# Kernel tuning notes

Measured on AMD Instinct MI355X. Metric: run time of the kernel, lower is better.

The kernel has to match this reference:

```python
import jax, jax.numpy as jnp
import numpy as np

N = 100000      # nodes
E = 3200000     # directed edges
F_IN = 128      # input node features
H = 16          # hidden width (fixed by module code)
C = 40          # classes
K_HOPS = 10
ALPHA = 0.1
BN_EPS = 1e-5


def gcn_conv(x, W, b, src, dst, n):
    """PyG GCNConv: add self-loops, symmetric D^-1/2 (A+I) D^-1/2 aggregation of x@W, plus bias."""
    loop = jnp.arange(n)
    s = jnp.concatenate([src, loop])
    d = jnp.concatenate([dst, loop])
    deg = jax.ops.segment_sum(jnp.ones(s.shape[0], x.dtype), d, num_segments=n)
    dinv = jnp.where(deg > 0, jax.lax.rsqrt(deg), 0.0)
    norm = dinv[s] * dinv[d]                      # [E+N]
    h = x @ W                                     # [N, out]
    out = jax.ops.segment_sum(h[s] * norm[:, None], d, num_segments=n)
    return out + b


def setup_inputs() -> dict:
    key = jax.random.key(0)
    ks = jax.random.split(key, 6)
    x = jax.random.normal(ks[0], (N, F_IN), jnp.float32)
    src = jax.random.randint(ks[1], (E,), 0, N)
    dst = jax.random.randint(ks[2], (E,), 0, N)
    glorot = lambda k, sh, fan: jax.random.normal(k, sh, jnp.float32) * np.float32(1.0 / np.sqrt(fan))
    W1 = glorot(ks[3], (F_IN, H), F_IN)
    b1 = jnp.zeros((H,), jnp.float32)
    gamma = jnp.ones((H,), jnp.float32)
    beta = jnp.zeros((H,), jnp.float32)
    Wl = glorot(ks[4], (H, H), H)
    bl = jnp.zeros((H,), jnp.float32)
    W2 = glorot(ks[5], (H, C), H)
    b2 = jnp.zeros((C,), jnp.float32)
    return dict(x=x, src=src, dst=dst, W1=W1, b1=b1, gamma=gamma, beta=beta,
                Wl=Wl, bl=bl, W2=W2, b2=b2)


def reference(x, src, dst, W1, b1, gamma, beta, Wl, bl, W2, b2):
    h = jax.nn.relu(gcn_conv(x, W1, b1, src, dst, N))
    # BatchNorm1d in training mode: biased batch statistics over nodes
    mean = h.mean(axis=0)
    var = h.var(axis=0)
    h = (h - mean) * jax.lax.rsqrt(var + BN_EPS) * gamma + beta
    # k_hops iterations of tiny linear-relu-residual blend
    def step(h, _):
        return ALPHA * jax.nn.relu(h @ Wl + bl) + (1.0 - ALPHA) * h, None
    h, _ = jax.lax.scan(step, h, None, length=K_HOPS)
    out = gcn_conv(h, W2, b2, src, dst, N)
    return jax.nn.log_softmax(out, axis=1)
```

## Files before the change

kernel.cpp:

```cpp
#include <hip/hip_runtime.h>
#include <hip/hip_fp16.h>
#include <math.h>

#define F_IN 128
#define H 16
#define C 40
#define K_HOPS 10
#define ALPHA 0.1f
#define BN_EPS 1e-5f

#define RB 256
#define RB_BITS 8
#define NBKT_MAX 512
#define SRC_MASK 0x1FFFF
#define PADQ 32
#define NDUMMY 2048
#define CAPB_BITS 14
#define CAPB (1 << CAPB_BITS)
#define STAGE_CAP 14336

typedef int v4i __attribute__((ext_vector_type(4)));

__global__ void k_zero(int* __restrict__ gcur, float* __restrict__ stats,
                       __half* __restrict__ h1h, __half* __restrict__ hh, int n) {
    int id = blockIdx.x * blockDim.x + threadIdx.x;
    if (id < NBKT_MAX) gcur[id] = id << CAPB_BITS;
    if (id < 32) stats[id] = 0.0f;
    int* z1 = (int*)(h1h + (size_t)n * H);
    int* z2 = (int*)(hh + (size_t)n * H);
    if (id < NDUMMY * H / 2) { z1[id] = 0; z2[id] = 0; }
}

#define BIN_CHUNK 2048
__global__ __launch_bounds__(256) void k_bin(const int* __restrict__ src,
                                             const int* __restrict__ dst,
                                             int* __restrict__ gcur,
                                             int* __restrict__ temp, int e) {
    __shared__ int hist[NBKT_MAX];
    __shared__ int lcur[NBKT_MAX];
    int t = threadIdx.x;
    hist[t] = 0; hist[t + 256] = 0;
    __syncthreads();
    int base = blockIdx.x * BIN_CHUNK;
    int ss[8], dd[8];
#pragma unroll
    for (int i = 0; i < 8; ++i) {
        int idx = base + i * 256 + t;
        if (idx < e) {
            ss[i] = src[idx]; dd[i] = dst[idx];
            atomicAdd(&hist[dd[i] >> RB_BITS], 1);
        } else ss[i] = -1;
    }
    __syncthreads();
    for (int b = t; b < NBKT_MAX; b += 256) {
        int hv = hist[b];
        lcur[b] = hv ? atomicAdd(&gcur[b], hv) : 0;
    }
    __syncthreads();
#pragma unroll
    for (int i = 0; i < 8; ++i) {
        if (ss[i] >= 0) {
            int d = dd[i];
            int b = d >> RB_BITS;
            int pos = atomicAdd(&lcur[b], 1);
            temp[pos] = ss[i] | ((d & (RB - 1)) << 17);
        }
    }
}

__global__ __launch_bounds__(256) void k_sort(const int* __restrict__ gcur,
                                              const int* __restrict__ temp,
                                              int* __restrict__ csr,
                                              int* __restrict__ ostart,
                                              int* __restrict__ oend,
                                              int* __restrict__ onode,
                                              float* __restrict__ dinv, int n) {
    __shared__ int hist[RB];
    __shared__ int cur[RB];
    __shared__ int psum[256];
    __shared__ int qh[64];
    __shared__ int qb[64];
    __shared__ int stage[STAGE_CAP];
    int t = threadIdx.x;
    int bkt = blockIdx.x;
    int start = bkt << CAPB_BITS;
    int endi = gcur[bkt];
    hist[t] = 0;
    if (t < 64) qh[t] = 0;
    __syncthreads();
    for (int k = start + t; k < endi; k += 2048) {
        int v[8];
#pragma unroll
        for (int i = 0; i < 8; ++i) { int ix = k + i * 256; v[i] = (ix < endi) ? temp[ix] : -1; }
#pragma unroll
        for (int i = 0; i < 8; ++i) if (v[i] >= 0) atomicAdd(&hist[v[i] >> 17], 1);
    }
    __syncthreads();
    int node = (bkt << RB_BITS) + t;
    int h = hist[t];
    int p = (h + PADQ - 1) & ~(PADQ - 1);
    bool va = (node < n);
    if (va) dinv[node] = rsqrtf((float)(h + 1));
    psum[t] = p;
    __syncthreads();
    for (int off = 1; off < 256; off <<= 1) {
        int tmp = (t >= off) ? psum[t - off] : 0;
        __syncthreads();
        psum[t] += tmp;
        __syncthreads();
    }
    int pexcl = psum[t] - p;
    int s0 = start + pexcl;
    int q = 63 - min(p >> 5, 63);
    int r = atomicAdd(&qh[q], 1);
    __syncthreads();
    int ptotal = psum[255];
    if (t == 0) {
        int run = 0;
        for (int i = 0; i < 64; ++i) { qb[i] = run; run += qh[i]; }
    }
    __syncthreads();
    int ga = (bkt << RB_BITS) + qb[q] + r;
    ostart[ga] = s0; oend[ga] = s0 + p; onode[ga] = va ? node : -1;

    if (ptotal <= STAGE_CAP) {
        cur[t] = pexcl;
        for (int i = t; i < ptotal; i += 256) stage[i] = -1;
        __syncthreads();
        for (int k = start + t; k < endi; k += 2048) {
            int v[8];
#pragma unroll
            for (int i = 0; i < 8; ++i) { int ix = k + i * 256; v[i] = (ix < endi) ? temp[ix] : -1; }
#pragma unroll
            for (int i = 0; i < 8; ++i) {
                if (v[i] >= 0) {
                    int pos = atomicAdd(&cur[v[i] >> 17], 1);
                    stage[pos] = v[i] & SRC_MASK;
                }
            }
        }
        __syncthreads();
        for (int i = t * 4; i < ptotal; i += 1024) {
            v4i v = *reinterpret_cast<const v4i*>(&stage[i]);
            int gi = start + i;
            v.x = (v.x < 0) ? n + ((gi + 0) & (NDUMMY - 1)) : v.x;
            v.y = (v.y < 0) ? n + ((gi + 1) & (NDUMMY - 1)) : v.y;
            v.z = (v.z < 0) ? n + ((gi + 2) & (NDUMMY - 1)) : v.z;
            v.w = (v.w < 0) ? n + ((gi + 3) & (NDUMMY - 1)) : v.w;
            *reinterpret_cast<v4i*>(&csr[gi]) = v;
        }
    } else {
        cur[t] = s0;
        __syncthreads();
        for (int k = start + t; k < endi; k += 256) {
            int v = temp[k];
            int pos = atomicAdd(&cur[v >> 17], 1);
            csr[pos] = v & SRC_MASK;
        }
        __syncthreads();
        for (int i = s0 + h; i < s0 + p; ++i) csr[i] = n + (i & (NDUMMY - 1));
    }
}

__global__ __launch_bounds__(256) void k_mm1(const float* __restrict__ x,
                                             const float* __restrict__ W1,
                                             const float* __restrict__ dinv,
                                             __half* __restrict__ h1h, int n) {
    __shared__ __align__(16) float xs[16 * 132];
    __shared__ __align__(16) float ws[128 * 16];
    int t = threadIdx.x;
    int node0 = blockIdx.x * 16;
    const float4* x4 = reinterpret_cast<const float4*>(x);
    const float4* w4 = reinterpret_cast<const float4*>(W1);
#pragma unroll
    for (int r = 0; r < 2; ++r) {
        int f = t + r * 256;
        int nl = f >> 5, k4 = f & 31;
        int nn = node0 + nl; if (nn >= n) nn = n - 1;
        *reinterpret_cast<float4*>(&xs[nl * 132 + k4 * 4]) = x4[(size_t)nn * 32 + k4];
        *reinterpret_cast<float4*>(&ws[f * 4]) = w4[f];
    }
    __syncthreads();
    int nl = t >> 4, j = t & 15;
    float acc = 0.0f;
#pragma unroll 8
    for (int k = 0; k < 128; ++k)
        acc = fmaf(xs[nl * 132 + k], ws[k * 16 + j], acc);
    int node = node0 + nl;
    if (node < n) h1h[(size_t)node * H + j] = __float2half(acc * dinv[node]);
}

__device__ __forceinline__ void acc8(float* a, int4 gv) {
    const __half2* h = reinterpret_cast<const __half2*>(&gv);
    float2 f0 = __half22float2(h[0]);
    float2 f1 = __half22float2(h[1]);
    float2 f2 = __half22float2(h[2]);
    float2 f3 = __half22float2(h[3]);
    a[0] += f0.x; a[1] += f0.y; a[2] += f1.x; a[3] += f1.y;
    a[4] += f2.x; a[5] += f2.y; a[6] += f3.x; a[7] += f3.y;
}

__global__ __launch_bounds__(256) void k_gather1(const int* __restrict__ ostart,
                                                 const int* __restrict__ oend,
                                                 const int* __restrict__ onode,
                                                 const int* __restrict__ csr,
                                                 const __half* __restrict__ h1h,
                                                 const float* __restrict__ dinv,
                                                 const float* __restrict__ b1,
                                                 float* __restrict__ hout,
                                                 float* __restrict__ stats, int n) {
    __shared__ float sm[32];
    __shared__ float b1s[16];
    int t = threadIdx.x;
    if (t < 32) sm[t] = 0.0f;
    if (t < 16) b1s[t] = b1[t];
    __syncthreads();
    int idx = blockIdx.x * 256 + t;
    int g = idx >> 2;
    int L = idx & 3, p = L >> 1, jj = L & 1;
    int node = __builtin_nontemporal_load(onode + g);
    float a[8];
#pragma unroll
    for (int k = 0; k < 8; ++k) a[k] = 0.0f;
    const int4* tab = reinterpret_cast<const int4*>(h1h);
    if (node >= 0) {
        int c  = (__builtin_nontemporal_load(ostart + g) >> 2) + (p << 2);
        int ce = __builtin_nontemporal_load(oend + g) >> 2;
        const v4i* csr4 = reinterpret_cast<const v4i*>(csr);
        for (; c < ce; c += 8) {
            v4i e0 = __builtin_nontemporal_load(csr4 + c);
            v4i e1 = __builtin_nontemporal_load(csr4 + c + 1);
            v4i e2 = __builtin_nontemporal_load(csr4 + c + 2);
            v4i e3 = __builtin_nontemporal_load(csr4 + c + 3);
            int4 g0  = tab[(size_t)e0.x * 2 + jj];
            int4 g1  = tab[(size_t)e0.y * 2 + jj];
            int4 g2  = tab[(size_t)e0.z * 2 + jj];
            int4 g3  = tab[(size_t)e0.w * 2 + jj];
            int4 g4  = tab[(size_t)e1.x * 2 + jj];
            int4 g5  = tab[(size_t)e1.y * 2 + jj];
            int4 g6  = tab[(size_t)e1.z * 2 + jj];
            int4 g7  = tab[(size_t)e1.w * 2 + jj];
            int4 g8  = tab[(size_t)e2.x * 2 + jj];
            int4 g9  = tab[(size_t)e2.y * 2 + jj];
            int4 g10 = tab[(size_t)e2.z * 2 + jj];
            int4 g11 = tab[(size_t)e2.w * 2 + jj];
            int4 g12 = tab[(size_t)e3.x * 2 + jj];
            int4 g13 = tab[(size_t)e3.y * 2 + jj];
            int4 g14 = tab[(size_t)e3.z * 2 + jj];
            int4 g15 = tab[(size_t)e3.w * 2 + jj];
            acc8(a, g0);  acc8(a, g1);  acc8(a, g2);  acc8(a, g3);
            acc8(a, g4);  acc8(a, g5);  acc8(a, g6);  acc8(a, g7);
            acc8(a, g8);  acc8(a, g9);  acc8(a, g10); acc8(a, g11);
            acc8(a, g12); acc8(a, g13); acc8(a, g14); acc8(a, g15);
        }
    }
#pragma unroll
    for (int k = 0; k < 8; ++k) a[k] += __shfl_xor(a[k], 2);
    float din = 0.0f;
    int4 sv = make_int4(0, 0, 0, 0);
    if (node >= 0) {
        din = dinv[node];
        sv = tab[(size_t)node * 2 + jj];
    }
    float v[8];
    {
        const __half2* h = reinterpret_cast<const __half2*>(&sv);
        float2 f0 = __half22float2(h[0]), f1 = __half22float2(h[1]);
        float2 f2 = __half22float2(h[2]), f3 = __half22float2(h[3]);
        float s8[8] = { f0.x, f0.y, f1.x, f1.y, f2.x, f2.y, f3.x, f3.y };
        bool writer = (node >= 0) && (p == 0);
#pragma unroll
        for (int k = 0; k < 8; ++k) {
            float val = fmaxf(din * (a[k] + s8[k]) + b1s[jj * 8 + k], 0.0f);
            v[k] = writer ? val : 0.0f;
        }
        if (writer) {
            float4* o = reinterpret_cast<float4*>(hout + (size_t)node * H + jj * 8);
            o[0] = make_float4(v[0], v[1], v[2], v[3]);
            o[1] = make_float4(v[4], v[5], v[6], v[7]);
        }
    }
#pragma unroll
    for (int k = 0; k < 8; ++k) {
        float s1 = v[k], s2 = v[k] * v[k];
        s1 += __shfl_xor(s1, 2);  s2 += __shfl_xor(s2, 2);
        s1 += __shfl_xor(s1, 4);  s2 += __shfl_xor(s2, 4);
        s1 += __shfl_xor(s1, 8);  s2 += __shfl_xor(s2, 8);
        s1 += __shfl_xor(s1, 16); s2 += __shfl_xor(s2, 16);
        s1 += __shfl_xor(s1, 32); s2 += __shfl_xor(s2, 32);
        if ((t & 63) < 2) {
            atomicAdd(&sm[jj * 8 + k], s1);
            atomicAdd(&sm[16 + jj * 8 + k], s2);
        }
    }
    __syncthreads();
    if (t < 32) atomicAdd(&stats[t], sm[t]);
}

__global__ void k_bncoef(float* __restrict__ stats, const float* __restrict__ gamma,
                         const float* __restrict__ beta, float nf) {
    int j = threadIdx.x;
    if (j < 16) {
        float mean = stats[j] / nf;
        float var = stats[16 + j] / nf - mean * mean;
        float a = gamma[j] * rsqrtf(var + BN_EPS);
        float c = beta[j] - mean * a;
        stats[j] = a;
        stats[16 + j] = c;
    }
}

__global__ __launch_bounds__(256) void k_hops(const float* __restrict__ h,
                                              __half* __restrict__ hh,
                                              const float* __restrict__ stats,
                                              const float* __restrict__ Wl,
                                              const float* __restrict__ bl,
                                              const float* __restrict__ dinv, int n) {
    __shared__ float wl[256], bls[16], av[16], cv[16];
    int t = threadIdx.x;
    wl[t] = Wl[(t & 15) * 16 + (t >> 4)];
    if (t < 16) { bls[t] = bl[t]; av[t] = stats[t]; cv[t] = stats[16 + t]; }
    __syncthreads();
    int node = blockIdx.x * 256 + t;
    if (node >= n) return;
    float hr[16];
    {
        const float4* hp = reinterpret_cast<const float4*>(h + (size_t)node * H);
        float4 v0 = hp[0], v1 = hp[1], v2 = hp[2], v3 = hp[3];
        hr[0] = v0.x; hr[1] = v0.y; hr[2] = v0.z; hr[3] = v0.w;
        hr[4] = v1.x; hr[5] = v1.y; hr[6] = v1.z; hr[7] = v1.w;
        hr[8] = v2.x; hr[9] = v2.y; hr[10] = v2.z; hr[11] = v2.w;
        hr[12] = v3.x; hr[13] = v3.y; hr[14] = v3.z; hr[15] = v3.w;
    }
#pragma unroll
    for (int j = 0; j < 16; ++j) hr[j] = hr[j] * av[j] + cv[j];
    for (int it = 0; it < K_HOPS; ++it) {
        float tmp[16];
#pragma unroll
        for (int j = 0; j < 16; ++j) {
            float a = bls[j];
#pragma unroll
            for (int k = 0; k < 16; ++k) a = fmaf(hr[k], wl[j * 16 + k], a);
            tmp[j] = fmaxf(a, 0.0f);
        }
#pragma unroll
        for (int j = 0; j < 16; ++j) hr[j] = ALPHA * tmp[j] + (1.0f - ALPHA) * hr[j];
    }
    {
        float din = dinv[node];
        __half2 ph[8];
#pragma unroll
        for (int i = 0; i < 8; ++i)
            ph[i] = __floats2half2_rn(hr[2 * i] * din, hr[2 * i + 1] * din);
        int4* hp = reinterpret_cast<int4*>(hh + (size_t)node * H);
        hp[0] = *reinterpret_cast<int4*>(&ph[0]);
        hp[1] = *reinterpret_cast<int4*>(&ph[4]);
    }
}

__global__ __launch_bounds__(256) void k_gather2(const int* __restrict__ ostart,
                                                 const int* __restrict__ oend,
                                                 const int* __restrict__ onode,
                                                 const int* __restrict__ csr,
                                                 const __half* __restrict__ hh,
                                                 const float* __restrict__ dinv,
                                                 float* __restrict__ agg, int n) {
    int t = threadIdx.x;
    int idx = blockIdx.x * 256 + t;
    int g = idx >> 2;
    int L = idx & 3, p = L >> 1, jj = L & 1;
    int node = __builtin_nontemporal_load(onode + g);
    float a[8];
#pragma unroll
    for (int k = 0; k < 8; ++k) a[k] = 0.0f;
    const int4* tab = reinterpret_cast<const int4*>(hh);
    if (node >= 0) {
        int c  = (__builtin_nontemporal_load(ostart + g) >> 2) + (p << 2);
        int ce = __builtin_nontemporal_load(oend + g) >> 2;
        const v4i* csr4 = reinterpret_cast<const v4i*>(csr);
        for (; c < ce; c += 8) {
            v4i e0 = __builtin_nontemporal_load(csr4 + c);
            v4i e1 = __builtin_nontemporal_load(csr4 + c + 1);
            v4i e2 = __builtin_nontemporal_load(csr4 + c + 2);
            v4i e3 = __builtin_nontemporal_load(csr4 + c + 3);
            int4 g0  = tab[(size_t)e0.x * 2 + jj];
            int4 g1  = tab[(size_t)e0.y * 2 + jj];
            int4 g2  = tab[(size_t)e0.z * 2 + jj];
            int4 g3  = tab[(size_t)e0.w * 2 + jj];
            int4 g4  = tab[(size_t)e1.x * 2 + jj];
            int4 g5  = tab[(size_t)e1.y * 2 + jj];
            int4 g6  = tab[(size_t)e1.z * 2 + jj];
            int4 g7  = tab[(size_t)e1.w * 2 + jj];
            int4 g8  = tab[(size_t)e2.x * 2 + jj];
            int4 g9  = tab[(size_t)e2.y * 2 + jj];
            int4 g10 = tab[(size_t)e2.z * 2 + jj];
            int4 g11 = tab[(size_t)e2.w * 2 + jj];
            int4 g12 = tab[(size_t)e3.x * 2 + jj];
            int4 g13 = tab[(size_t)e3.y * 2 + jj];
            int4 g14 = tab[(size_t)e3.z * 2 + jj];
            int4 g15 = tab[(size_t)e3.w * 2 + jj];
            acc8(a, g0);  acc8(a, g1);  acc8(a, g2);  acc8(a, g3);
            acc8(a, g4);  acc8(a, g5);  acc8(a, g6);  acc8(a, g7);
            acc8(a, g8);  acc8(a, g9);  acc8(a, g10); acc8(a, g11);
            acc8(a, g12); acc8(a, g13); acc8(a, g14); acc8(a, g15);
        }
    }
#pragma unroll
    for (int k = 0; k < 8; ++k) a[k] += __shfl_xor(a[k], 2);
    if (node >= 0 && p == 0) {
        float din = dinv[node];
        int4 sv = tab[(size_t)node * 2 + jj];
        const __half2* h = reinterpret_cast<const __half2*>(&sv);
        float2 f0 = __half22float2(h[0]), f1 = __half22float2(h[1]);
        float2 f2 = __half22float2(h[2]), f3 = __half22float2(h[3]);
        float s8[8] = { f0.x, f0.y, f1.x, f1.y, f2.x, f2.y, f3.x, f3.y };
        float v[8];
#pragma unroll
        for (int k = 0; k < 8; ++k) v[k] = din * (a[k] + s8[k]);
        float4* o = reinterpret_cast<float4*>(agg + (size_t)node * H + jj * 8);
        o[0] = make_float4(v[0], v[1], v[2], v[3]);
        o[1] = make_float4(v[4], v[5], v[6], v[7]);
    }
}

__global__ __launch_bounds__(256) void k_final(const float* __restrict__ agg2,
                                               const float* __restrict__ W2,
                                               const float* __restrict__ b2,
                                               float* __restrict__ out, int n) {
    __shared__ float w2s[16 * 40];
    __shared__ float b2s[40];
    __shared__ float ostage[40 * 257];
    int t = threadIdx.x;
    for (int i = t; i < 640; i += 256) w2s[i] = W2[i];
    if (t < 40) b2s[t] = b2[t];
    __syncthreads();
    int node = blockIdx.x * 256 + t;
    if (node < n) {
        float g[16];
        const float4* ap = reinterpret_cast<const float4*>(agg2 + (size_t)node * H);
#pragma unroll
        for (int r = 0; r < 4; ++r) {
            float4 a = ap[r];
            g[r * 4 + 0] = a.x; g[r * 4 + 1] = a.y; g[r * 4 + 2] = a.z; g[r * 4 + 3] = a.w;
        }
        float z[40];
#pragma unroll
        for (int j = 0; j < 40; ++j) {
            float a = b2s[j];
#pragma unroll
            for (int k = 0; k < 16; ++k) a = fmaf(g[k], w2s[k * 40 + j], a);
            z[j] = a;
        }
        float m = z[0];
#pragma unroll
        for (int j = 1; j < 40; ++j) m = fmaxf(m, z[j]);
        float s = 0.0f;
#pragma unroll
        for (int j = 0; j < 40; ++j) s += expf(z[j] - m);
        float lse = m + logf(s);
#pragma unroll
        for (int j = 0; j < 40; ++j) ostage[j * 257 + t] = z[j] - lse;
    }
    __syncthreads();
    int nodes = n - blockIdx.x * 256;
    if (nodes > 256) nodes = 256;
    int total = nodes * 40;
    size_t base = (size_t)blockIdx.x * 256 * 40;
    for (int i = t; i < total; i += 256) {
        int nl = i / 40;
        int j = i - nl * 40;
        out[base + i] = ostage[j * 257 + nl];
    }
}

extern "C" void kernel_launch(void* const* d_in, const int* in_sizes, int n_in,
                              void* d_out, int out_size, void* d_ws, size_t ws_size,
                              hipStream_t stream) {
    const float* x     = (const float*)d_in[0];
    const int*   src   = (const int*)d_in[1];
    const int*   dst   = (const int*)d_in[2];
    const float* W1    = (const float*)d_in[3];
    const float* b1    = (const float*)d_in[4];
    const float* gamma = (const float*)d_in[5];
    const float* beta  = (const float*)d_in[6];
    const float* Wl    = (const float*)d_in[7];
    const float* bl    = (const float*)d_in[8];
    const float* W2    = (const float*)d_in[9];
    const float* b2    = (const float*)d_in[10];
    float* out = (float*)d_out;

    int n = in_sizes[0] / F_IN;
    int e = in_sizes[1];
    int nbkt = (n + RB - 1) >> RB_BITS;
    int nAlign = (n + 15) & ~15;
    int nG = nbkt * RB;
    size_t bktB = (size_t)nbkt << CAPB_BITS;
    size_t hTileB = (size_t)nAlign * H * 4;
    size_t unionB = bktB * 4;
    if (unionB < 2 * hTileB) unionB = 2 * hTileB;

    char* wsb = (char*)d_ws;
    int*    csr      = (int*)wsb;      wsb += (bktB + 64) * 4;
    char*   uni      = wsb;            wsb += unionB;
    int*    temp     = (int*)uni;
    float*  hbuf     = (float*)uni;
    float*  agg2     = (float*)(uni + hTileB);
    int*    ostart   = (int*)wsb;      wsb += (size_t)(nG + 16) * 4;
    int*    oend     = (int*)wsb;      wsb += (size_t)(nG + 16) * 4;
    int*    onode    = (int*)wsb;      wsb += (size_t)(nG + 16) * 4;
    float*  dinv     = (float*)wsb;    wsb += (size_t)nAlign * 4;
    int*    gcur     = (int*)wsb;      wsb += NBKT_MAX * 4;
    float*  stats    = (float*)wsb;    wsb += 64 * 4;
    __half* h1h      = (__half*)wsb;   wsb += (size_t)(nAlign + NDUMMY + 16) * H * 2;
    __half* hh       = (__half*)wsb;   wsb += (size_t)(nAlign + NDUMMY + 16) * H * 2;

    k_zero<<<64, 256, 0, stream>>>(gcur, stats, h1h, hh, n);
    k_bin<<<(e + BIN_CHUNK - 1) / BIN_CHUNK, 256, 0, stream>>>(src, dst, gcur, temp, e);
    k_sort<<<nbkt, 256, 0, stream>>>(gcur, temp, csr, ostart, oend, onode, dinv, n);
    k_mm1<<<(n + 15) / 16, 256, 0, stream>>>(x, W1, dinv, h1h, n);
    k_gather1<<<nbkt * 4, 256, 0, stream>>>(ostart, oend, onode, csr, h1h, dinv, b1, hbuf, stats, n);
    k_bncoef<<<1, 16, 0, stream>>>(stats, gamma, beta, (float)n);
    k_hops<<<(n + 255) / 256, 256, 0, stream>>>(hbuf, hh, stats, Wl, bl, dinv, n);
    k_gather2<<<nbkt * 4, 256, 0, stream>>>(ostart, oend, onode, csr, hh, dinv, agg2, n);
    k_final<<<(n + 255) / 256, 256, 0, stream>>>(agg2, W2, b2, out, n);
}
```

Measured before the change: 299.6 us.

## Stage binned edges in LDS for coalesced scatter and vectorize sort reads

The binning kernel now processes 4096 edges per block with 16-byte vector loads, computes a block-local prefix sum over buckets, and stages the packed entries in shared memory sorted by bucket. It then writes them out contiguously per bucket to the global temp array instead of scattering each one individually. The sort kernel reads temp with v4i loads in both its histogram and staging passes. This is meant to cut uncoalesced global writes and load instruction count, at the cost of more shared memory per block (lower occupancy), an extra scan, and possible misalignment since temp+start vector loads assume 16-byte alignment.

```diff
diff --git a/kernel.cpp b/kernel.cpp
--- a/kernel.cpp
+++ b/kernel.cpp
@@ -31,40 +31,85 @@
     if (id < NDUMMY * H / 2) { z1[id] = 0; z2[id] = 0; }
 }
 
-#define BIN_CHUNK 2048
+#define BIN_CHUNK 4096
 __global__ __launch_bounds__(256) void k_bin(const int* __restrict__ src,
                                              const int* __restrict__ dst,
                                              int* __restrict__ gcur,
                                              int* __restrict__ temp, int e) {
     __shared__ int hist[NBKT_MAX];
-    __shared__ int lcur[NBKT_MAX];
+    __shared__ int runst[NBKT_MAX];
+    __shared__ int cur[NBKT_MAX];
+    __shared__ int gofs[NBKT_MAX];
+    __shared__ int psum[256];
+    __shared__ int stageV[BIN_CHUNK];
+    __shared__ unsigned short stageB[BIN_CHUNK];
     int t = threadIdx.x;
     hist[t] = 0; hist[t + 256] = 0;
     __syncthreads();
     int base = blockIdx.x * BIN_CHUNK;
-    int ss[8], dd[8];
-#pragma unroll
-    for (int i = 0; i < 8; ++i) {
-        int idx = base + i * 256 + t;
-        if (idx < e) {
-            ss[i] = src[idx]; dd[i] = dst[idx];
-            atomicAdd(&hist[dd[i] >> RB_BITS], 1);
-        } else ss[i] = -1;
-    }
-    __syncthreads();
-    for (int b = t; b < NBKT_MAX; b += 256) {
-        int hv = hist[b];
-        lcur[b] = hv ? atomicAdd(&gcur[b], hv) : 0;
-    }
-    __syncthreads();
-#pragma unroll
-    for (int i = 0; i < 8; ++i) {
-        if (ss[i] >= 0) {
-            int d = dd[i];
-            int b = d >> RB_BITS;
-            int pos = atomicAdd(&lcur[b], 1);
-            temp[pos] = ss[i] | ((d & (RB - 1)) << 17);
-        }
+    int cnt = e - base; if (cnt > BIN_CHUNK) cnt = BIN_CHUNK;
+    const v4i* s4 = reinterpret_cast<const v4i*>(src + base);
+    const v4i* d4 = reinterpret_cast<const v4i*>(dst + base);
+    v4i sv[4], dv[4];
+#pragma unroll
+    for (int i = 0; i < 4; ++i) {
+        int e0 = (t * 4 + i) * 4;
+        if (e0 + 3 < cnt) { sv[i] = s4[t * 4 + i]; dv[i] = d4[t * 4 + i]; }
+        else if (e0 < cnt) {
+            int ts[4], td[4];
+#pragma unroll
+            for (int j = 0; j < 4; ++j) {
+                int ei = e0 + j;
+                ts[j] = (ei < cnt) ? src[base + ei] : 0;
+                td[j] = (ei < cnt) ? dst[base + ei] : -1;
+            }
+            sv[i] = *reinterpret_cast<v4i*>(ts); dv[i] = *reinterpret_cast<v4i*>(td);
+        } else { dv[i] = (v4i){-1, -1, -1, -1}; sv[i] = dv[i]; }
+    }
+#pragma unroll
+    for (int i = 0; i < 4; ++i) {
+        if (dv[i].x >= 0) atomicAdd(&hist[dv[i].x >> RB_BITS], 1);
+        if (dv[i].y >= 0) atomicAdd(&hist[dv[i].y >> RB_BITS], 1);
+        if (dv[i].z >= 0) atomicAdd(&hist[dv[i].z >> RB_BITS], 1);
+        if (dv[i].w >= 0) atomicAdd(&hist[dv[i].w >> RB_BITS], 1);
+    }
+    __syncthreads();
+    int b0 = 2 * t, b1 = 2 * t + 1;
+    int h0 = hist[b0], h1 = hist[b1];
+    psum[t] = h0 + h1;
+    __syncthreads();
+    for (int off = 1; off < 256; off <<= 1) {
+        int tmp = (t >= off) ? psum[t - off] : 0;
+        __syncthreads();
+        psum[t] += tmp;
+        __syncthreads();
+    }
+    int excl = psum[t] - (h0 + h1);
+    runst[b0] = excl; runst[b1] = excl + h0;
+    int g0 = h0 ? atomicAdd(&gcur[b0], h0) : 0;
+    int g1 = h1 ? atomicAdd(&gcur[b1], h1) : 0;
+    gofs[b0] = g0 - excl; gofs[b1] = g1 - (excl + h0);
+    cur[b0] = excl; cur[b1] = excl + h0;
+    __syncthreads();
+#pragma unroll
+    for (int i = 0; i < 4; ++i) {
+        int ds[4] = { dv[i].x, dv[i].y, dv[i].z, dv[i].w };
+        int ssx[4] = { sv[i].x, sv[i].y, sv[i].z, sv[i].w };
+#pragma unroll
+        for (int j = 0; j < 4; ++j) {
+            int d = ds[j];
+            if (d >= 0) {
+                int b = d >> RB_BITS;
+                int pos = atomicAdd(&cur[b], 1);
+                stageV[pos] = ssx[j] | ((d & (RB - 1)) << 17);
+                stageB[pos] = (unsigned short)b;
+            }
+        }
+    }
+    __syncthreads();
+    for (int i = t; i < cnt; i += 256) {
+        int b = stageB[i];
+        temp[gofs[b] + i] = stageV[i];
     }
 }
 
@@ -85,16 +130,21 @@
     int bkt = blockIdx.x;
     int start = bkt << CAPB_BITS;
     int endi = gcur[bkt];
+    int nv = endi - start;
+    int n4 = nv >> 2;
+    const v4i* t4 = reinterpret_cast<const v4i*>(temp + start);
     hist[t] = 0;
     if (t < 64) qh[t] = 0;
     __syncthreads();
-    for (int k = start + t; k < endi; k += 2048) {
-        int v[8];
-#pragma unroll
-        for (int i = 0; i < 8; ++i) { int ix = k + i * 256; v[i] = (ix < endi) ? temp[ix] : -1; }
-#pragma unroll
-        for (int i = 0; i < 8; ++i) if (v[i] >= 0) atomicAdd(&hist[v[i] >> 17], 1);
-    }
+    for (int k = t; k < n4; k += 256) {
+        v4i v = t4[k];
+        atomicAdd(&hist[v.x >> 17], 1);
+        atomicAdd(&hist[v.y >> 17], 1);
+        atomicAdd(&hist[v.z >> 17], 1);
+        atomicAdd(&hist[v.w >> 17], 1);
+    }
+    for (int k = start + (n4 << 2) + t; k < endi; k += 256)
+        atomicAdd(&hist[temp[k] >> 17], 1);
     __syncthreads();
     int node = (bkt << RB_BITS) + t;
     int h = hist[t];
@@ -127,17 +177,17 @@
         cur[t] = pexcl;
         for (int i = t; i < ptotal; i += 256) stage[i] = -1;
         __syncthreads();
-        for (int k = start + t; k < endi; k += 2048) {
-            int v[8];
-#pragma unroll
-            for (int i = 0; i < 8; ++i) { int ix = k + i * 256; v[i] = (ix < endi) ? temp[ix] : -1; }
-#pragma unroll
-            for (int i = 0; i < 8; ++i) {
-                if (v[i] >= 0) {
-                    int pos = atomicAdd(&cur[v[i] >> 17], 1);
-                    stage[pos] = v[i] & SRC_MASK;
-                }
-            }
+        for (int k = t; k < n4; k += 256) {
+            v4i v = t4[k];
+            int p0 = atomicAdd(&cur[v.x >> 17], 1); stage[p0] = v.x & SRC_MASK;
+            int p1 = atomicAdd(&cur[v.y >> 17], 1); stage[p1] = v.y & SRC_MASK;
+            int p2 = atomicAdd(&cur[v.z >> 17], 1); stage[p2] = v.z & SRC_MASK;
+            int p3 = atomicAdd(&cur[v.w >> 17], 1); stage[p3] = v.w & SRC_MASK;
+        }
+        for (int k = start + (n4 << 2) + t; k < endi; k += 256) {
+            int v = temp[k];
+            int pos = atomicAdd(&cur[v >> 17], 1);
+            stage[pos] = v & SRC_MASK;
         }
         __syncthreads();
         for (int i = t * 4; i < ptotal; i += 1024) {
```

Result: faster. 286.8 us (-4.3%).
